# Kernel tuning notes

Hardware: AMD Instinct MI355X
Metric: run time of the kernel (lower is better)

Reference implementation:

```python
import jax, jax.numpy as jnp
import numpy as np

N, H, E, D, L = 100000, 20000, 1600000, 64, 3
F = 4 * D  # ffn hidden = out_dim * 4


def _ln(x, g, b, eps=1e-5):
    mu = x.mean(-1, keepdims=True)
    var = ((x - mu) ** 2).mean(-1, keepdims=True)
    return (x - mu) * jax.lax.rsqrt(var + eps) * g + b


def _gconv(x, W, b, src, dst, inv_sqrt_src, inv_sqrt_dst, n_dst):
    # DGL GraphConv, norm='both': D_dst^{-1/2} A D_src^{-1/2} (x W) + b
    h = (x * inv_sqrt_src[:, None]) @ W
    agg = jax.ops.segment_sum(h[src], dst, num_segments=n_dst)
    return agg * inv_sqrt_dst[:, None] + b


def setup_inputs() -> dict:
    key = jax.random.key(0)
    ks = jax.random.split(key, 24)
    s = 0.05
    inp = {
        'node_features': jax.random.normal(ks[0], (N, D), jnp.float32),
        'edge_src': jax.random.randint(ks[1], (E,), 0, N),
        'edge_dst': jax.random.randint(ks[2], (E,), 0, H),
        'n_hyper': H,
        # stacked per-layer params [L, ...]
        'Wn2h': jax.random.normal(ks[3], (L, D, D), jnp.float32) * s,
        'bn2h': jnp.zeros((L, D), jnp.float32),
        'Wh2n': jax.random.normal(ks[4], (L, D, D), jnp.float32) * s,
        'bh2n': jnp.zeros((L, D), jnp.float32),
        'W1': jax.random.normal(ks[5], (L, D, F), jnp.float32) * s,
        'b1': jnp.zeros((L, F), jnp.float32),
        'W2': jax.random.normal(ks[6], (L, F, D), jnp.float32) * s,
        'b2': jnp.zeros((L, D), jnp.float32),
        'g1': jnp.ones((L, D), jnp.float32),
        'be1': jnp.zeros((L, D), jnp.float32),
        'g2': jnp.ones((L, D), jnp.float32),
        'be2': jnp.zeros((L, D), jnp.float32),
        'gF': jnp.ones((D,), jnp.float32),
        'bF': jnp.zeros((D,), jnp.float32),
        'Wo': jax.random.normal(ks[7], (D, D), jnp.float32) * s,
        'bo': jnp.zeros((D,), jnp.float32),
    }
    return inp


def reference(node_features, edge_src, edge_dst, n_hyper, Wn2h, bn2h, Wh2n, bh2n,
              W1, b1, W2, b2, g1, be1, g2, be2, gF, bF, Wo, bo):
    n_nodes = node_features.shape[0]
    ones = jnp.ones(edge_src.shape[0], node_features.dtype)
    deg_node = jnp.clip(jax.ops.segment_sum(ones, edge_src, num_segments=n_nodes), 1.0)
    deg_hyp = jnp.clip(jax.ops.segment_sum(ones, edge_dst, num_segments=n_hyper), 1.0)
    is_node = jax.lax.rsqrt(deg_node)  # node out-degree^{-1/2}
    is_hyp = jax.lax.rsqrt(deg_hyp)    # hyperedge in-degree^{-1/2}

    def step(h, p):
        Wa, ba, Wb, bb, w1, c1, w2, c2, gg1, ee1, gg2, ee2 = p
        # node -> hyperedge conv (unused attention output is overwritten in the original)
        h_hyper = _gconv(h, Wa, ba, edge_src, edge_dst, is_node, is_hyp, n_hyper)
        # hyperedge -> node conv on reversed graph (degrees swap roles)
        h_node = _gconv(h_hyper, Wb, bb, edge_dst, edge_src, is_hyp, is_node, n_nodes)
        h = _ln(h + h_node, gg1, ee1)
        h_ffn = jax.nn.relu(h @ w1 + c1) @ w2 + c2
        h = _ln(h + h_ffn, gg2, ee2)
        return h, None

    h, _ = jax.lax.scan(step, node_features,
                        (Wn2h, bn2h, Wh2n, bh2n, W1, b1, W2, b2, g1, be1, g2, be2))
    h = _ln(h, gF, bF)
    return h @ Wo + bo
```

## Files before the change

### kernel.cpp

```cpp
#include <hip/hip_runtime.h>

#define HYP 20000
#define NLAYER 3
#define NB_H 313
#define NB_N 391
#define PT 4096

typedef __attribute__((ext_vector_type(8))) short short8;
typedef __attribute__((ext_vector_type(4))) float floatx4;

static __device__ __forceinline__ unsigned short f2bf(float f){
  union { float f; unsigned u; } v; v.f = f;
  unsigned r = v.u + 0x7FFF + ((v.u >> 16) & 1);
  return (unsigned short)(r >> 16);
}

__global__ __launch_bounds__(256) void k_hist(const int* __restrict__ src,
    const int* __restrict__ dst, int E, int* __restrict__ bh, int* __restrict__ bn){
  __shared__ int lh[NB_H + NB_N];
  int tid = threadIdx.x;
  for (int i = tid; i < NB_H + NB_N; i += 256) lh[i] = 0;
  __syncthreads();
  for (int i = blockIdx.x*256 + tid; i < E; i += gridDim.x*256){
    atomicAdd(&lh[dst[i] >> 6], 1);
    atomicAdd(&lh[NB_H + (src[i] >> 8)], 1);
  }
  __syncthreads();
  for (int i = tid; i < NB_H; i += 256) if (lh[i]) atomicAdd(&bh[i], lh[i]);
  for (int i = tid; i < NB_N; i += 256) if (lh[NB_H+i]) atomicAdd(&bn[i], lh[NB_H+i]);
}

__global__ __launch_bounds__(256) void k_bscan(const int* __restrict__ bh,
    const int* __restrict__ bn, int* __restrict__ bstart_h, int* __restrict__ gcur_h,
    int* __restrict__ bstart_n, int* __restrict__ gcur_n){
  __shared__ int ssc[4];
  __shared__ int scarry;
  int tid = threadIdx.x, lane = tid & 63, wv = tid >> 6;
  if (tid == 0) scarry = 0;
  __syncthreads();
  for (int base = 0; base < NB_H; base += 256){
    int i = base + tid; int v = (i < NB_H) ? bh[i] : 0; int x = v;
    #pragma unroll
    for (int o = 1; o < 64; o <<= 1){ int t = __shfl_up(x,o,64); if (lane >= o) x += t; }
    if (lane == 63) ssc[wv] = x;
    __syncthreads();
    int add = (wv>0?ssc[0]:0)+(wv>1?ssc[1]:0)+(wv>2?ssc[2]:0);
    int c = scarry;
    if (i < NB_H){ int ex = c + add + x - v; bstart_h[i] = ex; gcur_h[i] = ex; }
    __syncthreads();
    if (tid == 255) scarry = c + ssc[0]+ssc[1]+ssc[2]+ssc[3];
    __syncthreads();
  }
  if (tid == 0){ bstart_h[NB_H] = scarry; scarry = 0; }
  __syncthreads();
  for (int base = 0; base < NB_N; base += 256){
    int i = base + tid; int v = (i < NB_N) ? bn[i] : 0; int x = v;
    #pragma unroll
    for (int o = 1; o < 64; o <<= 1){ int t = __shfl_up(x,o,64); if (lane >= o) x += t; }
    if (lane == 63) ssc[wv] = x;
    __syncthreads();
    int add = (wv>0?ssc[0]:0)+(wv>1?ssc[1]:0)+(wv>2?ssc[2]:0);
    int c = scarry;
    if (i < NB_N){ int ex = c + add + x - v; bstart_n[i] = ex; gcur_n[i] = ex; }
    __syncthreads();
    if (tid == 255) scarry = c + ssc[0]+ssc[1]+ssc[2]+ssc[3];
    __syncthreads();
  }
  if (tid == 0) bstart_n[NB_N] = scarry;
}

__global__ __launch_bounds__(256) void k_partition2(
    const int* __restrict__ esrc, const int* __restrict__ edst, int E, int nblk,
    int* __restrict__ gcur_h, unsigned* __restrict__ Ebuf_h,
    int* __restrict__ gcur_n, unsigned* __restrict__ Ebuf_n){
  __shared__ unsigned sst[PT];
  __shared__ int lh[NB_N], lpre[NB_N], gb[NB_N];
  __shared__ int ssc[4];
  __shared__ int scarry;
  int tid = threadIdx.x, lane = tid & 63, wv = tid >> 6;
  bool hside = (blockIdx.x < nblk);
  int bb = hside ? blockIdx.x : blockIdx.x - nblk;
  const int* keys = hside ? edst : esrc;
  const int* pays = hside ? esrc : edst;
  int keyshift = hside ? 17 : 15;
  int nb = hside ? NB_H : NB_N;
  int* gcur = hside ? gcur_h : gcur_n;
  unsigned* Ebuf = hside ? Ebuf_h : Ebuf_n;

  int base = bb*PT;
  int m = min(PT, E - base);
  for (int i = tid; i < nb; i += 256) lh[i] = 0;
  if (tid == 0) scarry = 0;
  __syncthreads();
  unsigned en[16]; int rk[16];
  #pragma unroll
  for (int j = 0; j < 16; ++j){
    int i = base + j*256 + tid;
    if (i < E){
      unsigned k = (unsigned)keys[i], p = (unsigned)pays[i];
      en[j] = (k << keyshift) | p;
      rk[j] = atomicAdd(&lh[en[j] >> 23], 1);
    } else { en[j] = 0; rk[j] = -1; }
  }
  __syncthreads();
  for (int b2 = 0; b2 < nb; b2 += 256){
    int i = b2 + tid; int v = (i < nb) ? lh[i] : 0; int x = v;
    #pragma unroll
    for (int o = 1; o < 64; o <<= 1){ int t = __shfl_up(x,o,64); if (lane >= o) x += t; }
    if (lane == 63) ssc[wv] = x;
    __syncthreads();
    int add = (wv>0?ssc[0]:0)+(wv>1?ssc[1]:0)+(wv>2?ssc[2]:0);
    int c = scarry;
    if (i < nb) lpre[i] = c + add + x - v;
    __syncthreads();
    if (tid == 255) scarry = c + ssc[0]+ssc[1]+ssc[2]+ssc[3];
    __syncthreads();
  }
  for (int i = tid; i < nb; i += 256) gb[i] = atomicAdd(&gcur[i], lh[i]);
  #pragma unroll
  for (int j = 0; j < 16; ++j){
    if (rk[j] >= 0){
      int bk = en[j] >> 23;
      sst[lpre[bk] + rk[j]] = en[j];
    }
  }
  __syncthreads();
  for (int j = tid; j < m; j += 256){
    unsigned e = sst[j];
    int bk = e >> 23;
    Ebuf[gb[bk] + (j - lpre[bk])] = e;
  }
}

__global__ __launch_bounds__(256) void k_build2(
    const unsigned* __restrict__ Ebuf_h, const int* __restrict__ bstart_h,
    const unsigned* __restrict__ Ebuf_n, const int* __restrict__ bstart_n,
    int* __restrict__ off_h, float* __restrict__ is_h, int* __restrict__ csr_h,
    int* __restrict__ off_n, float* __restrict__ is_n, int* __restrict__ csr_n,
    const float* __restrict__ nf, unsigned short* __restrict__ xb,
    int Hn, int Nn){
  __shared__ int lcnt[256], lpre2[256], lcur[256];
  int tid = threadIdx.x, lane = tid & 63, wv = tid >> 6;
  bool hside = (blockIdx.x < NB_H);
  int b = hside ? blockIdx.x : blockIdx.x - NB_H;
  const unsigned* Ebuf = hside ? Ebuf_h : Ebuf_n;
  const int* bstart = hside ? bstart_h : bstart_n;
  int keyshift = hside ? 17 : 15;
  int ipb = hside ? 64 : 256;
  int paymask = hside ? 0x1FFFF : 0x7FFF;
  int limit = hside ? Hn : Nn;
  int* off = hside ? off_h : off_n;
  float* isv = hside ? is_h : is_n;
  int* csr = hside ? csr_h : csr_n;

  int base = bstart[b], m = bstart[b+1] - base;
  for (int i = tid; i < ipb; i += 256) lcnt[i] = 0;
  __syncthreads();
  for (int i = tid; i < m; i += 256){
    unsigned e = Ebuf[base + i];
    atomicAdd(&lcnt[(e >> keyshift) & (ipb-1)], 1);
  }
  __syncthreads();
  if (wv == 0){
    int carry = 0;
    for (int c = 0; c < ipb; c += 64){
      int li = c + lane;
      int v = lcnt[li]; int x = v;
      #pragma unroll
      for (int o = 1; o < 64; o <<= 1){ int t = __shfl_up(x,o,64); if (lane >= o) x += t; }
      int ex = carry + x - v;
      int id = b*ipb + li;
      if (id <= limit) off[id] = base + ex;
      if (id < limit) isv[id] = rsqrtf((float)(v > 0 ? v : 1));
      lpre2[li] = ex;
      carry += __shfl(x, 63, 64);
    }
  }
  for (int i = tid; i < ipb; i += 256) lcur[i] = 0;
  __syncthreads();
  for (int i = tid; i < m; i += 256){
    unsigned e = Ebuf[base + i];
    int li = (e >> keyshift) & (ipb-1);
    int pos = base + lpre2[li] + atomicAdd(&lcur[li], 1);
    csr[pos] = (int)(e & (unsigned)paymask);
  }
  if (!hside){
    int nbase = b*256;
    for (int i = tid; i < 2048; i += 256){
      int li = i >> 3, kc = (i & 7)*8;
      int id = nbase + li;
      if (id < Nn){
        int v = lcnt[li];
        float s = rsqrtf((float)(v > 0 ? v : 1));
        float4 v0 = *(const float4*)&nf[(size_t)id*64 + kc];
        float4 v1 = *(const float4*)&nf[(size_t)id*64 + kc + 4];
        uint4 o;
        o.x = (unsigned)f2bf(v0.x*s) | ((unsigned)f2bf(v0.y*s) << 16);
        o.y = (unsigned)f2bf(v0.z*s) | ((unsigned)f2bf(v0.w*s) << 16);
        o.z = (unsigned)f2bf(v1.x*s) | ((unsigned)f2bf(v1.y*s) << 16);
        o.w = (unsigned)f2bf(v1.z*s) | ((unsigned)f2bf(v1.w*s) << 16);
        *(uint4*)&xb[(size_t)id*64 + kc] = o;
      }
    }
  }
}

__global__ void k_cvtall(const float* __restrict__ W1, const float* __restrict__ W2,
                         const float* __restrict__ Wa, const float* __restrict__ Wb,
                         const float* __restrict__ Wo,
                         unsigned short* __restrict__ W1T, unsigned short* __restrict__ W2T,
                         unsigned short* __restrict__ WaT, unsigned short* __restrict__ WbT,
                         unsigned short* __restrict__ WoT){
  int st = gridDim.x*blockDim.x;
  int t0 = blockIdx.x*blockDim.x + threadIdx.x;
  for (int j = t0; j < NLAYER*16384; j += st){
    int l = j >> 14, n = (j >> 6) & 255, k = j & 63;
    W1T[j] = f2bf(W1[l*16384 + k*256 + n]);
  }
  for (int j = t0; j < NLAYER*16384; j += st){
    int l = j >> 14, o = (j >> 8) & 63, kk = j & 255;
    W2T[j] = f2bf(W2[l*16384 + kk*64 + o]);
  }
  for (int j = t0; j < NLAYER*4096; j += st){
    int l = j >> 12, n = (j >> 6) & 63, k = j & 63;
    WaT[j] = f2bf(Wa[l*4096 + k*64 + n]);
  }
  for (int j = t0; j < NLAYER*4096; j += st){
    int l = j >> 12, n = (j >> 6) & 63, k = j & 63;
    WbT[j] = f2bf(Wb[l*4096 + k*64 + n]);
  }
  for (int j = t0; j < 4096; j += st){
    int n = (j >> 6) & 63, k = j & 63;
    WoT[j] = f2bf(Wo[k*64 + n]);
  }
}

template<int LSTR>
static __device__ __forceinline__ void stage64(const unsigned short* __restrict__ gsrc,
    unsigned short* __restrict__ ldst, int tid, int rows){
  int nch = rows*8;
  for (int idx = tid; idx < nch; idx += 256){
    int row = idx >> 3, kc = (idx & 7)*8;
    uint4 v = *(const uint4*)&gsrc[row*64 + kc];
    *(uint4*)&ldst[row*LSTR + kc] = v;
  }
}

static __device__ __forceinline__ short8 rdswz(const unsigned short* __restrict__ l,
    int row, int slot){
  return *(const short8*)&l[(row << 6) + ((((unsigned)(slot ^ row)) & 7u) << 3)];
}

#define ACC8(u) \
  a0 += __uint_as_float(u.x << 16); a1 += __uint_as_float(u.x & 0xFFFF0000u); \
  a2 += __uint_as_float(u.y << 16); a3 += __uint_as_float(u.y & 0xFFFF0000u); \
  a4 += __uint_as_float(u.z << 16); a5 += __uint_as_float(u.z & 0xFFFF0000u); \
  a6 += __uint_as_float(u.w << 16); a7 += __uint_as_float(u.w & 0xFFFF0000u);

#define ACCV(u) \
  a[0] += __uint_as_float(u.x << 16); a[1] += __uint_as_float(u.x & 0xFFFF0000u); \
  a[2] += __uint_as_float(u.y << 16); a[3] += __uint_as_float(u.y & 0xFFFF0000u); \
  a[4] += __uint_as_float(u.z << 16); a[5] += __uint_as_float(u.z & 0xFFFF0000u); \
  a[6] += __uint_as_float(u.w << 16); a[7] += __uint_as_float(u.w & 0xFFFF0000u);

__global__ __launch_bounds__(256) void k_gather8(const unsigned short* __restrict__ feat,
    const int* __restrict__ csr, const int* __restrict__ off,
    unsigned short* __restrict__ agg, int nrows){
  int lane = threadIdx.x & 63, wvi = threadIdx.x >> 6;
  int g = lane >> 3;
  int ch = (lane & 7) * 8;
  int r = blockIdx.x*4 + wvi, stride = gridDim.x*4;
  for (; r < nrows; r += stride){
    int b = off[r], e = off[r+1];
    float a0=0,a1=0,a2=0,a3=0,a4=0,a5=0,a6=0,a7=0;
    int t = b;
    for (; t + 32 <= e; t += 32){
      int s0 = csr[t + g];
      int s1 = csr[t + 8 + g];
      int s2 = csr[t + 16 + g];
      int s3 = csr[t + 24 + g];
      uint4 u0 = *(const uint4*)&feat[(size_t)s0*64 + ch];
      uint4 u1 = *(const uint4*)&feat[(size_t)s1*64 + ch];
      uint4 u2 = *(const uint4*)&feat[(size_t)s2*64 + ch];
      uint4 u3 = *(const uint4*)&feat[(size_t)s3*64 + ch];
      ACC8(u0); ACC8(u1); ACC8(u2); ACC8(u3);
    }
    for (; t + 16 <= e; t += 16){
      int s0 = csr[t + g];
      int s1 = csr[t + 8 + g];
      uint4 u0 = *(const uint4*)&feat[(size_t)s0*64 + ch];
      uint4 u1 = *(const uint4*)&feat[(size_t)s1*64 + ch];
      ACC8(u0); ACC8(u1);
    }
    for (; t < e; t += 8){
      int idx = t + g;
      bool valid = idx < e;
      int s = csr[valid ? idx : b];
      uint4 u = *(const uint4*)&feat[(size_t)s*64 + ch];
      if (!valid){ u.x = 0; u.y = 0; u.z = 0; u.w = 0; }
      ACC8(u);
    }
    #pragma unroll
    for (int o = 8; o <= 32; o <<= 1){
      a0 += __shfl_xor(a0,o,64); a1 += __shfl_xor(a1,o,64);
      a2 += __shfl_xor(a2,o,64); a3 += __shfl_xor(a3,o,64);
      a4 += __shfl_xor(a4,o,64); a5 += __shfl_xor(a5,o,64);
      a6 += __shfl_xor(a6,o,64); a7 += __shfl_xor(a7,o,64);
    }
    if (g == 0){
      uint4 w;
      w.x = (unsigned)f2bf(a0) | ((unsigned)f2bf(a1) << 16);
      w.y = (unsigned)f2bf(a2) | ((unsigned)f2bf(a3) << 16);
      w.z = (unsigned)f2bf(a4) | ((unsigned)f2bf(a5) << 16);
      w.w = (unsigned)f2bf(a6) | ((unsigned)f2bf(a7) << 16);
      *(uint4*)&agg[(size_t)r*64 + ch] = w;
    }
  }
}

__global__ __launch_bounds__(256) void k_gatherN(const unsigned short* __restrict__ feat,
    const int* __restrict__ csr, const int* __restrict__ off,
    unsigned short* __restrict__ agg, int nrows){
  int lane = threadIdx.x & 63, wvi = threadIdx.x >> 6;
  int g = lane >> 3;
  int ch = (lane & 7) * 8;
  int wid = blockIdx.x*4 + wvi;
  int nw = gridDim.x*4;
  for (int r0 = wid*8; r0 < nrows; r0 += nw*8){
    int r = r0 + g;
    bool vr = (r < nrows);
    int b = 0, e = 0;
    if (vr){ b = off[r]; e = off[r+1]; }
    float a[8] = {0,0,0,0,0,0,0,0};
    int t = b;
    for (; t + 2 <= e; t += 2){
      int s0 = csr[t];
      int s1 = csr[t+1];
      uint4 u0 = *(const uint4*)&feat[(size_t)s0*64 + ch];
      uint4 u1 = *(const uint4*)&feat[(size_t)s1*64 + ch];
      ACCV(u0); ACCV(u1);
    }
    if (t < e){
      int s = csr[t];
      uint4 u = *(const uint4*)&feat[(size_t)s*64 + ch];
      ACCV(u);
    }
    if (vr){
      uint4 w;
      w.x = (unsigned)f2bf(a[0]) | ((unsigned)f2bf(a[1]) << 16);
      w.y = (unsigned)f2bf(a[2]) | ((unsigned)f2bf(a[3]) << 16);
      w.z = (unsigned)f2bf(a[4]) | ((unsigned)f2bf(a[5]) << 16);
      w.w = (unsigned)f2bf(a[6]) | ((unsigned)f2bf(a[7]) << 16);
      *(uint4*)&agg[(size_t)r*64 + ch] = w;
    }
  }
}

__global__ __launch_bounds__(64) void k_mmA(const unsigned short* __restrict__ aggb,
    const unsigned short* __restrict__ WaT, const float* __restrict__ bias,
    const float* __restrict__ ihy, unsigned short* __restrict__ ouths, int nrows){
  __shared__ unsigned short sWb[64*72];
  int lane = threadIdx.x;
  int quad = lane >> 4, n16 = lane & 15;
  for (int idx = lane; idx < 512; idx += 64){
    int row = idx >> 3, kc = (idx & 7)*8;
    *(uint4*)&sWb[row*72 + kc] = *(const uint4*)&WaT[row*64 + kc];
  }
  __syncthreads();
  int rowbase = blockIdx.x*16;
  int arow = min(rowbase + n16, nrows-1);
  short8 a0 = *(const short8*)&aggb[(size_t)arow*64 + quad*8];
  short8 a1 = *(const short8*)&aggb[(size_t)arow*64 + 32 + quad*8];
  float ih[4];
  #pragma unroll
  for (int r = 0; r < 4; ++r) ih[r] = ihy[min(rowbase + quad*4 + r, nrows-1)];
  #pragma unroll
  for (int ot = 0; ot < 4; ++ot){
    floatx4 c = (floatx4){0.f,0.f,0.f,0.f};
    short8 b0 = *(const short8*)&sWb[(ot*16+n16)*72 + quad*8];
    short8 b1 = *(const short8*)&sWb[(ot*16+n16)*72 + 32 + quad*8];
    c = __builtin_amdgcn_mfma_f32_16x16x32_bf16(a0, b0, c, 0, 0, 0);
    c = __builtin_amdgcn_mfma_f32_16x16x32_bf16(a1, b1, c, 0, 0, 0);
    float bl = bias[ot*16 + n16];
    #pragma unroll
    for (int r = 0; r < 4; ++r){
      int rr = rowbase + quad*4 + r;
      if (rr < nrows)
        ouths[(size_t)rr*64 + ot*16 + n16] = f2bf(fmaf(c[r], ih[r], bl) * ih[r]);
    }
  }
}

__global__ __launch_bounds__(1024) void k_fused(
    const unsigned short* __restrict__ aggb,
    const unsigned short* __restrict__ WbT,
    const float* __restrict__ bbg,
    const float* __restrict__ isn,
    const float* __restrict__ hin,
    const float* __restrict__ g1v, const float* __restrict__ be1v,
    const unsigned short* __restrict__ W1T, const float* __restrict__ b1g,
    const unsigned short* __restrict__ W2T, const float* __restrict__ b2g,
    const float* __restrict__ g2v, const float* __restrict__ be2v,
    float* __restrict__ Outp, unsigned short* __restrict__ Qs, int nrows)
{
  __shared__ unsigned short sWb[64*64];
  __shared__ unsigned short sW1[4*64*64];
  __shared__ unsigned short sW2[4*64*64];
  __shared__ unsigned short sPH[16*16*72];
  int tid = threadIdx.x;
  int lane = tid & 63, w = tid >> 6;
  int quad = lane >> 4, n16 = lane & 15;
  unsigned short* myP = &sPH[w*16*72];

  for (int c = tid; c < 4608; c += 1024){
    int tile = c >> 9, cc = c & 511;
    int row = cc >> 3, s = cc & 7;
    const unsigned short* src; unsigned short* dst; int gs;
    if (tile == 0){ src = WbT; gs = 64; dst = sWb; }
    else if (tile < 5){ int q = tile-1; src = W1T + q*64*64; gs = 64; dst = sW1 + q*4096; }
    else { int q = tile-5; src = W2T + q*64; gs = 256; dst = sW2 + q*4096; }
    uint4 v = *(const uint4*)&src[row*gs + s*8];
    *(uint4*)&dst[(row << 6) + ((((unsigned)(s ^ row)) & 7u) << 3)] = v;
  }

  float bbv[4], g1l[4], be1l[4], b2v[4], g2l[4], be2l[4];
  #pragma unroll
  for (int ot = 0; ot < 4; ++ot){
    bbv[ot] = bbg[ot*16 + n16];
    g1l[ot] = g1v[ot*16 + n16];  be1l[ot] = be1v[ot*16 + n16];
    b2v[ot] = b2g[ot*16 + n16];
    g2l[ot] = g2v[ot*16 + n16];  be2l[ot] = be2v[ot*16 + n16];
  }
  float b1v[4][4];
  #pragma unroll
  for (int q = 0; q < 4; ++q)
    #pragma unroll
    for (int c2 = 0; c2 < 4; ++c2)
      b1v[q][c2] = b1g[q*64 + c2*16 + n16];

  __syncthreads();

  int ngrp = (nrows + 15) >> 4;
  int wwid = blockIdx.x*16 + w;
  int nw = gridDim.x*16;

  for (int grp = wwid; grp < ngrp; grp += nw){
    int rb = grp*16;

    int arow = min(rb + n16, nrows-1);
    short8 a0 = *(const short8*)&aggb[(size_t)arow*64 + quad*8];
    short8 a1 = *(const short8*)&aggb[(size_t)arow*64 + 32 + quad*8];

    float pP[4][4];
    float isr[4];
    #pragma unroll
    for (int r = 0; r < 4; ++r) isr[r] = isn[min(rb + quad*4 + r, nrows-1)];
    #pragma unroll
    for (int ot = 0; ot < 4; ++ot){
      floatx4 c = (floatx4){0.f,0.f,0.f,0.f};
      short8 b0 = rdswz(sWb, ot*16+n16, quad);
      short8 b1 = rdswz(sWb, ot*16+n16, 4+quad);
      c = __builtin_amdgcn_mfma_f32_16x16x32_bf16(a0, b0, c, 0, 0, 0);
      c = __builtin_amdgcn_mfma_f32_16x16x32_bf16(a1, b1, c, 0, 0, 0);
      #pragma unroll
      for (int r = 0; r < 4; ++r){
        int rr = min(rb + quad*4 + r, nrows-1);
        pP[ot][r] = fmaf(c[r], isr[r], bbv[ot]) + hin[(size_t)rr*64 + ot*16 + n16];
      }
    }
    #pragma unroll
    for (int r = 0; r < 4; ++r){
      float sv = (pP[0][r] + pP[1][r]) + (pP[2][r] + pP[3][r]);
      float q = fmaf(pP[0][r], pP[0][r], pP[1][r]*pP[1][r]) +
                fmaf(pP[2][r], pP[2][r], pP[3][r]*pP[3][r]);
      #pragma unroll
      for (int o = 8; o >= 1; o >>= 1){
        sv += __shfl_xor(sv, o, 64);
        q  += __shfl_xor(q, o, 64);
      }
      float mu = sv*(1.f/64.f);
      float var = fmaf(-mu, mu, q*(1.f/64.f));
      float rs = rsqrtf(var + 1e-5f);
      #pragma unroll
      for (int ot = 0; ot < 4; ++ot)
        pP[ot][r] = fmaf((pP[ot][r]-mu)*rs, g1l[ot], be1l[ot]);
    }
    #pragma unroll
    for (int ot = 0; ot < 4; ++ot)
      #pragma unroll
      for (int r = 0; r < 4; ++r)
        myP[(quad*4 + r)*72 + ot*16 + n16] = f2bf(pP[ot][r]);
    short8 p0 = *(const short8*)&myP[n16*72 + quad*8];
    short8 p1 = *(const short8*)&myP[n16*72 + 32 + quad*8];

    floatx4 acc2[4];
    #pragma unroll
    for (int t = 0; t < 4; ++t) acc2[t] = (floatx4){0.f,0.f,0.f,0.f};

    #pragma unroll
    for (int q = 0; q < 4; ++q){
      const unsigned short* sA = sW1 + q*4096;
      const unsigned short* sB = sW2 + q*4096;
      #pragma unroll
      for (int ck2 = 0; ck2 < 2; ++ck2){
        #pragma unroll
        for (int nt = 0; nt < 2; ++nt){
          int nl = ck2*32 + nt*16 + n16;
          floatx4 c = (floatx4){0.f,0.f,0.f,0.f};
          short8 b0 = rdswz(sA, nl, quad);
          short8 b1f = rdswz(sA, nl, 4+quad);
          c = __builtin_amdgcn_mfma_f32_16x16x32_bf16(p0, b0, c, 0, 0, 0);
          c = __builtin_amdgcn_mfma_f32_16x16x32_bf16(p1, b1f, c, 0, 0, 0);
          float bb = b1v[q][ck2*2 + nt];
          #pragma unroll
          for (int r = 0; r < 4; ++r){
            float h = fmaxf(c[r] + bb, 0.f);
            myP[(quad*4 + r)*40 + nt*16 + n16] = f2bf(h);
          }
        }
        short8 a2 = *(const short8*)&myP[n16*40 + quad*8];
        #pragma unroll
        for (int ot = 0; ot < 4; ++ot){
          short8 b2f = rdswz(sB, ot*16+n16, ck2*4 + quad);
          acc2[ot] = __builtin_amdgcn_mfma_f32_16x16x32_bf16(a2, b2f, acc2[ot], 0, 0, 0);
        }
      }
    }

    float pre[4][4];
    #pragma unroll
    for (int ot = 0; ot < 4; ++ot)
      #pragma unroll
      for (int r = 0; r < 4; ++r)
        pre[ot][r] = acc2[ot][r] + b2v[ot] + pP[ot][r];
    #pragma unroll
    for (int r = 0; r < 4; ++r){
      float sv = (pre[0][r] + pre[1][r]) + (pre[2][r] + pre[3][r]);
      float q = fmaf(pre[0][r], pre[0][r], pre[1][r]*pre[1][r]) +
                fmaf(pre[2][r], pre[2][r], pre[3][r]*pre[3][r]);
      #pragma unroll
      for (int o = 8; o >= 1; o >>= 1){
        sv += __shfl_xor(sv, o, 64);
        q  += __shfl_xor(q, o, 64);
      }
      float mu = sv*(1.f/64.f);
      float var = fmaf(-mu, mu, q*(1.f/64.f));
      float rs = rsqrtf(var + 1e-5f);
      int rr = rb + quad*4 + r;
      if (rr < nrows){
        float isr2 = isn[rr];
        #pragma unroll
        for (int ot = 0; ot < 4; ++ot){
          float ov = fmaf((pre[ot][r]-mu)*rs, g2l[ot], be2l[ot]);
          Outp[(size_t)rr*64 + ot*16 + n16] = ov;
          Qs[(size_t)rr*64 + ot*16 + n16] = f2bf(ov * isr2);
        }
      }
    }
  }
}

__global__ __launch_bounds__(256) void k_final(const float* __restrict__ Q,
    const unsigned short* __restrict__ WoT, const float* __restrict__ bog,
    const float* __restrict__ gF, const float* __restrict__ bF,
    float* __restrict__ out, int nrows){
  __shared__ unsigned short sWb[64*72];
  int tid = threadIdx.x;
  int lane = tid & 63, w = tid >> 6;
  int quad = lane >> 4, n16 = lane & 15;
  stage64<72>(WoT, sWb, tid, 64);
  __syncthreads();
  int rowbase = blockIdx.x*64 + w*16;
  int arow = min(rowbase + n16, nrows-1);
  float4 q0 = *(const float4*)&Q[(size_t)arow*64 + quad*8];
  float4 q1 = *(const float4*)&Q[(size_t)arow*64 + quad*8 + 4];
  float4 q2 = *(const float4*)&Q[(size_t)arow*64 + 32 + quad*8];
  float4 q3 = *(const float4*)&Q[(size_t)arow*64 + 32 + quad*8 + 4];
  float s = (q0.x+q0.y+q0.z+q0.w) + (q1.x+q1.y+q1.z+q1.w)
          + (q2.x+q2.y+q2.z+q2.w) + (q3.x+q3.y+q3.z+q3.w);
  float qq = (q0.x*q0.x+q0.y*q0.y+q0.z*q0.z+q0.w*q0.w)
           + (q1.x*q1.x+q1.y*q1.y+q1.z*q1.z+q1.w*q1.w)
           + (q2.x*q2.x+q2.y*q2.y+q2.z*q2.z+q2.w*q2.w)
           + (q3.x*q3.x+q3.y*q3.y+q3.z*q3.z+q3.w*q3.w);
  s += __shfl_xor(s, 16, 64);  qq += __shfl_xor(qq, 16, 64);
  s += __shfl_xor(s, 32, 64);  qq += __shfl_xor(qq, 32, 64);
  float mu = s*(1.f/64.f);
  float var = fmaf(-mu, mu, qq*(1.f/64.f));
  float rs = rsqrtf(var + 1e-5f);
  float4 g0 = *(const float4*)&gF[quad*8];
  float4 g1 = *(const float4*)&gF[quad*8 + 4];
  float4 g2 = *(const float4*)&gF[32 + quad*8];
  float4 g3 = *(const float4*)&gF[32 + quad*8 + 4];
  float4 f0 = *(const float4*)&bF[quad*8];
  float4 f1 = *(const float4*)&bF[quad*8 + 4];
  float4 f2 = *(const float4*)&bF[32 + quad*8];
  float4 f3 = *(const float4*)&bF[32 + quad*8 + 4];
  short8 a0, a1;
  a0[0]=f2bf(fmaf((q0.x-mu)*rs, g0.x, f0.x)); a0[1]=f2bf(fmaf((q0.y-mu)*rs, g0.y, f0.y));
  a0[2]=f2bf(fmaf((q0.z-mu)*rs, g0.z, f0.z)); a0[3]=f2bf(fmaf((q0.w-mu)*rs, g0.w, f0.w));
  a0[4]=f2bf(fmaf((q1.x-mu)*rs, g1.x, f1.x)); a0[5]=f2bf(fmaf((q1.y-mu)*rs, g1.y, f1.y));
  a0[6]=f2bf(fmaf((q1.z-mu)*rs, g1.z, f1.z)); a0[7]=f2bf(fmaf((q1.w-mu)*rs, g1.w, f1.w));
  a1[0]=f2bf(fmaf((q2.x-mu)*rs, g2.x, f2.x)); a1[1]=f2bf(fmaf((q2.y-mu)*rs, g2.y, f2.y));
  a1[2]=f2bf(fmaf((q2.z-mu)*rs, g2.z, f2.z)); a1[3]=f2bf(fmaf((q2.w-mu)*rs, g2.w, f2.w));
  a1[4]=f2bf(fmaf((q3.x-mu)*rs, g3.x, f3.x)); a1[5]=f2bf(fmaf((q3.y-mu)*rs, g3.y, f3.y));
  a1[6]=f2bf(fmaf((q3.z-mu)*rs, g3.z, f3.z)); a1[7]=f2bf(fmaf((q3.w-mu)*rs, g3.w, f3.w));
  #pragma unroll
  for (int ot = 0; ot < 4; ++ot){
    floatx4 c = (floatx4){0.f,0.f,0.f,0.f};
    short8 b0 = *(const short8*)&sWb[(ot*16+n16)*72 + quad*8];
    short8 b1 = *(const short8*)&sWb[(ot*16+n16)*72 + 32 + quad*8];
    c = __builtin_amdgcn_mfma_f32_16x16x32_bf16(a0, b0, c, 0, 0, 0);
    c = __builtin_amdgcn_mfma_f32_16x16x32_bf16(a1, b1, c, 0, 0, 0);
    float bol = bog[ot*16 + n16];
    #pragma unroll
    for (int r = 0; r < 4; ++r){
      int rr = rowbase + quad*4 + r;
      if (rr < nrows) out[(size_t)rr*64 + ot*16 + n16] = c[r] + bol;
    }
  }
}

extern "C" void kernel_launch(void* const* d_in, const int* in_sizes, int n_in,
                              void* d_out, int out_size, void* d_ws, size_t ws_size,
                              hipStream_t stream){
  const float* nf   = (const float*)d_in[0];
  const int*   esrc = (const int*)d_in[1];
  const int*   edst = (const int*)d_in[2];
  const float* Wn2h = (const float*)d_in[4];
  const float* bn2h = (const float*)d_in[5];
  const float* Wh2n = (const float*)d_in[6];
  const float* bh2n = (const float*)d_in[7];
  const float* W1   = (const float*)d_in[8];
  const float* b1   = (const float*)d_in[9];
  const float* W2   = (const float*)d_in[10];
  const float* b2   = (const float*)d_in[11];
  const float* g1   = (const float*)d_in[12];
  const float* be1  = (const float*)d_in[13];
  const float* g2   = (const float*)d_in[14];
  const float* be2  = (const float*)d_in[15];
  const float* gF   = (const float*)d_in[16];
  const float* bF   = (const float*)d_in[17];
  const float* Wo   = (const float*)d_in[18];
  const float* bo   = (const float*)d_in[19];
  const int N = in_sizes[0] / 64;
  const int E = in_sizes[1];
  const int H = HYP;
  float* out = (float*)d_out;

  char* w = (char*)d_ws;
  auto carve = [&](size_t bytes) -> char* {
    char* p = w; w += (bytes + 255) & ~(size_t)255; return p;
  };
  int* bh = (int*)carve((size_t)(NB_H + NB_N)*4);
  int* bn = bh + NB_H;
  int* bstart_h = (int*)carve((size_t)(NB_H+1)*4);
  int* gcur_h   = (int*)carve((size_t)NB_H*4);
  int* bstart_n = (int*)carve((size_t)(NB_N+1)*4);
  int* gcur_n   = (int*)carve((size_t)NB_N*4);
  unsigned* Ebuf_h = (unsigned*)carve((size_t)E*4);
  unsigned* Ebuf_n = (unsigned*)carve((size_t)E*4);
  int*   off_h = (int*)carve((size_t)(H+1)*4);
  int*   off_n = (int*)carve((size_t)(N+1)*4);
  float* is_h  = (float*)carve((size_t)H*4);
  float* is_n  = (float*)carve((size_t)N*4);
  int*   csr_h = (int*)carve((size_t)E*4);
  int*   csr_n = (int*)carve((size_t)E*4);
  unsigned short* aggxb = (unsigned short*)carve((size_t)H*64*2);
  unsigned short* agghb = (unsigned short*)carve((size_t)N*64*2);
  float* Qb    = (float*)carve((size_t)N*64*4);
  unsigned short* hhsb = (unsigned short*)carve((size_t)H*64*2);
  unsigned short* xb0  = (unsigned short*)carve((size_t)N*64*2);
  unsigned short* Qs   = (unsigned short*)carve((size_t)N*64*2);
  unsigned short* W1g16 = (unsigned short*)carve((size_t)NLAYER*64*256*2);
  unsigned short* W2g16 = (unsigned short*)carve((size_t)NLAYER*256*64*2);
  unsigned short* Wag16 = (unsigned short*)carve((size_t)NLAYER*4096*2);
  unsigned short* Wbg16 = (unsigned short*)carve((size_t)NLAYER*4096*2);
  unsigned short* Wog16 = (unsigned short*)carve((size_t)4096*2);

  hipMemsetAsync(bh, 0, (size_t)(NB_H + NB_N)*4, stream);
  k_cvtall<<<96, 256, 0, stream>>>(W1, W2, Wn2h, Wh2n, Wo,
                                   W1g16, W2g16, Wag16, Wbg16, Wog16);
  k_hist<<<512, 256, 0, stream>>>(esrc, edst, E, bh, bn);
  k_bscan<<<1, 256, 0, stream>>>(bh, bn, bstart_h, gcur_h, bstart_n, gcur_n);
  const int nblk = (E + PT - 1)/PT;
  k_partition2<<<2*nblk, 256, 0, stream>>>(esrc, edst, E, nblk,
                                           gcur_h, Ebuf_h, gcur_n, Ebuf_n);
  k_build2<<<NB_H + NB_N, 256, 0, stream>>>(Ebuf_h, bstart_h, Ebuf_n, bstart_n,
                                            off_h, is_h, csr_h,
                                            off_n, is_n, csr_n,
                                            nf, xb0, H, N);

  const int NB64 = (N + 63)/64;
  const int HB16 = (H + 15)/16;
  for (int l = 0; l < NLAYER; ++l){
    const float* hin = (l == 0) ? nf : Qb;
    const unsigned short* hsrc = (l == 0) ? xb0 : Qs;
    k_gather8<<<2048, 256, 0, stream>>>(hsrc, csr_h, off_h, aggxb, H);
    k_mmA<<<HB16, 64, 0, stream>>>(aggxb, Wag16 + l*4096, bn2h + l*64, is_h, hhsb, H);
    k_gatherN<<<2048, 256, 0, stream>>>(hhsb, csr_n, off_n, agghb, N);
    k_fused<<<256, 1024, 0, stream>>>(agghb, Wbg16 + l*4096, bh2n + l*64, is_n, hin,
                                      g1 + l*64, be1 + l*64,
                                      W1g16 + l*64*256, b1 + l*256,
                                      W2g16 + l*256*64, b2 + l*64,
                                      g2 + l*64, be2 + l*64, Qb, Qs, N);
  }
  k_final<<<NB64, 256, 0, stream>>>(Qb, Wog16, bo, gF, bF, out, N);
}
```

Before: 457.4 us.

## Fuse both GraphConv weight matmuls into the hyperedge gather kernel

Since aggregation is linear, the hyperedge-to-node weight Wb is applied per hyperedge before the node-side gather instead of after it. The new gather kernel also applies Wa, the bias and the degree scaling with scalar FMAs against LDS-held bf16 weights. This removes the separate k_mmA launch, its bf16 intermediate and the Wb MFMA in k_fused, and Wa/Wb are no longer pre-converted in k_cvtall. In exchange the hyperedge output is stored as fp32, so the heavy node-side gather reads twice as many bytes per edge. Every gather block also converts both weight matrices into LDS, and k_fused now reads bf16 aggregates with scalar 2-byte loads.

```diff
diff --git a/kernel.cpp b/kernel.cpp
--- a/kernel.cpp
+++ b/kernel.cpp
@@ -206,10 +206,8 @@
 }
 
 __global__ void k_cvtall(const float* __restrict__ W1, const float* __restrict__ W2,
-                         const float* __restrict__ Wa, const float* __restrict__ Wb,
                          const float* __restrict__ Wo,
                          unsigned short* __restrict__ W1T, unsigned short* __restrict__ W2T,
-                         unsigned short* __restrict__ WaT, unsigned short* __restrict__ WbT,
                          unsigned short* __restrict__ WoT){
   int st = gridDim.x*blockDim.x;
   int t0 = blockIdx.x*blockDim.x + threadIdx.x;
@@ -220,14 +218,6 @@
   for (int j = t0; j < NLAYER*16384; j += st){
     int l = j >> 14, o = (j >> 8) & 63, kk = j & 255;
     W2T[j] = f2bf(W2[l*16384 + kk*64 + o]);
-  }
-  for (int j = t0; j < NLAYER*4096; j += st){
-    int l = j >> 12, n = (j >> 6) & 63, k = j & 63;
-    WaT[j] = f2bf(Wa[l*4096 + k*64 + n]);
-  }
-  for (int j = t0; j < NLAYER*4096; j += st){
-    int l = j >> 12, n = (j >> 6) & 63, k = j & 63;
-    WbT[j] = f2bf(Wb[l*4096 + k*64 + n]);
   }
   for (int j = t0; j < 4096; j += st){
     int n = (j >> 6) & 63, k = j & 63;
@@ -251,28 +241,51 @@
   return *(const short8*)&l[(row << 6) + ((((unsigned)(slot ^ row)) & 7u) << 3)];
 }
 
-#define ACC8(u) \
-  a0 += __uint_as_float(u.x << 16); a1 += __uint_as_float(u.x & 0xFFFF0000u); \
-  a2 += __uint_as_float(u.y << 16); a3 += __uint_as_float(u.y & 0xFFFF0000u); \
-  a4 += __uint_as_float(u.z << 16); a5 += __uint_as_float(u.z & 0xFFFF0000u); \
-  a6 += __uint_as_float(u.w << 16); a7 += __uint_as_float(u.w & 0xFFFF0000u);
-
 #define ACCV(u) \
   a[0] += __uint_as_float(u.x << 16); a[1] += __uint_as_float(u.x & 0xFFFF0000u); \
   a[2] += __uint_as_float(u.y << 16); a[3] += __uint_as_float(u.y & 0xFFFF0000u); \
   a[4] += __uint_as_float(u.z << 16); a[5] += __uint_as_float(u.z & 0xFFFF0000u); \
   a[6] += __uint_as_float(u.w << 16); a[7] += __uint_as_float(u.w & 0xFFFF0000u);
 
-__global__ __launch_bounds__(256) void k_gather8(const unsigned short* __restrict__ feat,
-    const int* __restrict__ csr, const int* __restrict__ off,
-    unsigned short* __restrict__ agg, int nrows){
-  int lane = threadIdx.x & 63, wvi = threadIdx.x >> 6;
-  int g = lane >> 3;
-  int ch = (lane & 7) * 8;
+#define ACCF(ua, ub) \
+  a[0] += ua.x; a[1] += ua.y; a[2] += ua.z; a[3] += ua.w; \
+  a[4] += ub.x; a[5] += ub.y; a[6] += ub.z; a[7] += ub.w;
+
+#define MV8(acc, s, wv_) \
+  acc[0] = fmaf(s, __uint_as_float(wv_.x << 16), acc[0]); \
+  acc[1] = fmaf(s, __uint_as_float(wv_.x & 0xFFFF0000u), acc[1]); \
+  acc[2] = fmaf(s, __uint_as_float(wv_.y << 16), acc[2]); \
+  acc[3] = fmaf(s, __uint_as_float(wv_.y & 0xFFFF0000u), acc[3]); \
+  acc[4] = fmaf(s, __uint_as_float(wv_.z << 16), acc[4]); \
+  acc[5] = fmaf(s, __uint_as_float(wv_.z & 0xFFFF0000u), acc[5]); \
+  acc[6] = fmaf(s, __uint_as_float(wv_.w << 16), acc[6]); \
+  acc[7] = fmaf(s, __uint_as_float(wv_.w & 0xFFFF0000u), acc[7]);
+
+__global__ __launch_bounds__(256) void k_gatherHW(
+    const unsigned short* __restrict__ feat, const int* __restrict__ csr,
+    const int* __restrict__ off, const float* __restrict__ Waf,
+    const float* __restrict__ bav_g, const float* __restrict__ Wbf,
+    const float* __restrict__ ihy, float* __restrict__ zb, int nrows){
+  __shared__ unsigned short sWa[64*72];
+  __shared__ unsigned short sWb[64*72];
+  int tid = threadIdx.x;
+  for (int idx = tid; idx < 4096; idx += 256){
+    int k = idx >> 6, j = idx & 63;
+    sWa[k*72 + j] = f2bf(Waf[idx]);
+    sWb[k*72 + j] = f2bf(Wbf[idx]);
+  }
+  int lane = tid & 63, wvi = tid >> 6;
+  int g = lane >> 3, i8 = lane & 7;
+  int ch = i8*8;
+  float bav[8];
+  #pragma unroll
+  for (int m = 0; m < 8; ++m) bav[m] = bav_g[g*8 + m];
+  __syncthreads();
+
   int r = blockIdx.x*4 + wvi, stride = gridDim.x*4;
   for (; r < nrows; r += stride){
     int b = off[r], e = off[r+1];
-    float a0=0,a1=0,a2=0,a3=0,a4=0,a5=0,a6=0,a7=0;
+    float a[8] = {0,0,0,0,0,0,0,0};
     int t = b;
     for (; t + 32 <= e; t += 32){
       int s0 = csr[t + g];
@@ -283,14 +296,14 @@
       uint4 u1 = *(const uint4*)&feat[(size_t)s1*64 + ch];
       uint4 u2 = *(const uint4*)&feat[(size_t)s2*64 + ch];
       uint4 u3 = *(const uint4*)&feat[(size_t)s3*64 + ch];
-      ACC8(u0); ACC8(u1); ACC8(u2); ACC8(u3);
+      ACCV(u0); ACCV(u1); ACCV(u2); ACCV(u3);
     }
     for (; t + 16 <= e; t += 16){
       int s0 = csr[t + g];
       int s1 = csr[t + 8 + g];
       uint4 u0 = *(const uint4*)&feat[(size_t)s0*64 + ch];
       uint4 u1 = *(const uint4*)&feat[(size_t)s1*64 + ch];
-      ACC8(u0); ACC8(u1);
+      ACCV(u0); ACCV(u1);
     }
     for (; t < e; t += 8){
       int idx = t + g;
@@ -298,27 +311,51 @@
       int s = csr[valid ? idx : b];
       uint4 u = *(const uint4*)&feat[(size_t)s*64 + ch];
       if (!valid){ u.x = 0; u.y = 0; u.z = 0; u.w = 0; }
-      ACC8(u);
+      ACCV(u);
     }
     #pragma unroll
     for (int o = 8; o <= 32; o <<= 1){
-      a0 += __shfl_xor(a0,o,64); a1 += __shfl_xor(a1,o,64);
-      a2 += __shfl_xor(a2,o,64); a3 += __shfl_xor(a3,o,64);
-      a4 += __shfl_xor(a4,o,64); a5 += __shfl_xor(a5,o,64);
-      a6 += __shfl_xor(a6,o,64); a7 += __shfl_xor(a7,o,64);
+      #pragma unroll
+      for (int m = 0; m < 8; ++m) a[m] += __shfl_xor(a[m], o, 64);
+    }
+    float ih = ihy[r];
+    float p[8] = {0,0,0,0,0,0,0,0};
+    #pragma unroll
+    for (int tt = 0; tt < 8; ++tt){
+      uint4 wv_ = *(const uint4*)&sWa[(i8*8 + tt)*72 + g*8];
+      float at = a[tt];
+      MV8(p, at, wv_);
+    }
+    #pragma unroll
+    for (int o = 1; o <= 4; o <<= 1){
+      #pragma unroll
+      for (int m = 0; m < 8; ++m) p[m] += __shfl_xor(p[m], o, 64);
+    }
+    float hh[8];
+    #pragma unroll
+    for (int m = 0; m < 8; ++m) hh[m] = fmaf(p[m], ih, bav[m]) * ih;
+    float q[8] = {0,0,0,0,0,0,0,0};
+    #pragma unroll
+    for (int tt = 0; tt < 8; ++tt){
+      uint4 wv_ = *(const uint4*)&sWb[(g*8 + tt)*72 + i8*8];
+      float ht = hh[tt];
+      MV8(q, ht, wv_);
+    }
+    #pragma unroll
+    for (int o = 8; o <= 32; o <<= 1){
+      #pragma unroll
+      for (int m = 0; m < 8; ++m) q[m] += __shfl_xor(q[m], o, 64);
     }
     if (g == 0){
-      uint4 w;
-      w.x = (unsigned)f2bf(a0) | ((unsigned)f2bf(a1) << 16);
-      w.y = (unsigned)f2bf(a2) | ((unsigned)f2bf(a3) << 16);
-      w.z = (unsigned)f2bf(a4) | ((unsigned)f2bf(a5) << 16);
-      w.w = (unsigned)f2bf(a6) | ((unsigned)f2bf(a7) << 16);
-      *(uint4*)&agg[(size_t)r*64 + ch] = w;
-    }
-  }
-}
-
-__global__ __launch_bounds__(256) void k_gatherN(const unsigned short* __restrict__ feat,
+      float4 w0; w0.x = q[0]; w0.y = q[1]; w0.z = q[2]; w0.w = q[3];
+      float4 w1; w1.x = q[4]; w1.y = q[5]; w1.z = q[6]; w1.w = q[7];
+      *(float4*)&zb[(size_t)r*64 + ch] = w0;
+      *(float4*)&zb[(size_t)r*64 + ch + 4] = w1;
+    }
+  }
+}
+
+__global__ __launch_bounds__(256) void k_gatherN(const float* __restrict__ feat,
     const int* __restrict__ csr, const int* __restrict__ off,
     unsigned short* __restrict__ agg, int nrows){
   int lane = threadIdx.x & 63, wvi = threadIdx.x >> 6;
@@ -336,14 +373,17 @@
     for (; t + 2 <= e; t += 2){
       int s0 = csr[t];
       int s1 = csr[t+1];
-      uint4 u0 = *(const uint4*)&feat[(size_t)s0*64 + ch];
-      uint4 u1 = *(const uint4*)&feat[(size_t)s1*64 + ch];
-      ACCV(u0); ACCV(u1);
+      float4 u0a = *(const float4*)&feat[(size_t)s0*64 + ch];
+      float4 u0b = *(const float4*)&feat[(size_t)s0*64 + ch + 4];
+      float4 u1a = *(const float4*)&feat[(size_t)s1*64 + ch];
+      float4 u1b = *(const float4*)&feat[(size_t)s1*64 + ch + 4];
+      ACCF(u0a, u0b); ACCF(u1a, u1b);
     }
     if (t < e){
       int s = csr[t];
-      uint4 u = *(const uint4*)&feat[(size_t)s*64 + ch];
-      ACCV(u);
+      float4 ua = *(const float4*)&feat[(size_t)s*64 + ch];
+      float4 ub = *(const float4*)&feat[(size_t)s*64 + ch + 4];
+      ACCF(ua, ub);
     }
     if (vr){
       uint4 w;
@@ -356,44 +396,8 @@
   }
 }
 
-__global__ __launch_bounds__(64) void k_mmA(const unsigned short* __restrict__ aggb,
-    const unsigned short* __restrict__ WaT, const float* __restrict__ bias,
-    const float* __restrict__ ihy, unsigned short* __restrict__ ouths, int nrows){
-  __shared__ unsigned short sWb[64*72];
-  int lane = threadIdx.x;
-  int quad = lane >> 4, n16 = lane & 15;
-  for (int idx = lane; idx < 512; idx += 64){
-    int row = idx >> 3, kc = (idx & 7)*8;
-    *(uint4*)&sWb[row*72 + kc] = *(const uint4*)&WaT[row*64 + kc];
-  }
-  __syncthreads();
-  int rowbase = blockIdx.x*16;
-  int arow = min(rowbase + n16, nrows-1);
-  short8 a0 = *(const short8*)&aggb[(size_t)arow*64 + quad*8];
-  short8 a1 = *(const short8*)&aggb[(size_t)arow*64 + 32 + quad*8];
-  float ih[4];
-  #pragma unroll
-  for (int r = 0; r < 4; ++r) ih[r] = ihy[min(rowbase + quad*4 + r, nrows-1)];
-  #pragma unroll
-  for (int ot = 0; ot < 4; ++ot){
-    floatx4 c = (floatx4){0.f,0.f,0.f,0.f};
-    short8 b0 = *(const short8*)&sWb[(ot*16+n16)*72 + quad*8];
-    short8 b1 = *(const short8*)&sWb[(ot*16+n16)*72 + 32 + quad*8];
-    c = __builtin_amdgcn_mfma_f32_16x16x32_bf16(a0, b0, c, 0, 0, 0);
-    c = __builtin_amdgcn_mfma_f32_16x16x32_bf16(a1, b1, c, 0, 0, 0);
-    float bl = bias[ot*16 + n16];
-    #pragma unroll
-    for (int r = 0; r < 4; ++r){
-      int rr = rowbase + quad*4 + r;
-      if (rr < nrows)
-        ouths[(size_t)rr*64 + ot*16 + n16] = f2bf(fmaf(c[r], ih[r], bl) * ih[r]);
-    }
-  }
-}
-
 __global__ __launch_bounds__(1024) void k_fused(
     const unsigned short* __restrict__ aggb,
-    const unsigned short* __restrict__ WbT,
     const float* __restrict__ bbg,
     const float* __restrict__ isn,
     const float* __restrict__ hin,
@@ -403,7 +407,6 @@
     const float* __restrict__ g2v, const float* __restrict__ be2v,
     float* __restrict__ Outp, unsigned short* __restrict__ Qs, int nrows)
 {
-  __shared__ unsigned short sWb[64*64];
   __shared__ unsigned short sW1[4*64*64];
   __shared__ unsigned short sW2[4*64*64];
   __shared__ unsigned short sPH[16*16*72];
@@ -412,13 +415,12 @@
   int quad = lane >> 4, n16 = lane & 15;
   unsigned short* myP = &sPH[w*16*72];
 
-  for (int c = tid; c < 4608; c += 1024){
+  for (int c = tid; c < 4096; c += 1024){
     int tile = c >> 9, cc = c & 511;
     int row = cc >> 3, s = cc & 7;
     const unsigned short* src; unsigned short* dst; int gs;
-    if (tile == 0){ src = WbT; gs = 64; dst = sWb; }
-    else if (tile < 5){ int q = tile-1; src = W1T + q*64*64; gs = 64; dst = sW1 + q*4096; }
-    else { int q = tile-5; src = W2T + q*64; gs = 256; dst = sW2 + q*4096; }
+    if (tile < 4){ src = W1T + tile*64*64; gs = 64; dst = sW1 + tile*4096; }
+    else { int q = tile-4; src = W2T + q*64; gs = 256; dst = sW2 + q*4096; }
     uint4 v = *(const uint4*)&src[row*gs + s*8];
     *(uint4*)&dst[(row << 6) + ((((unsigned)(s ^ row)) & 7u) << 3)] = v;
   }
@@ -447,25 +449,17 @@
   for (int grp = wwid; grp < ngrp; grp += nw){
     int rb = grp*16;
 
-    int arow = min(rb + n16, nrows-1);
-    short8 a0 = *(const short8*)&aggb[(size_t)arow*64 + quad*8];
-    short8 a1 = *(const short8*)&aggb[(size_t)arow*64 + 32 + quad*8];
-
     float pP[4][4];
     float isr[4];
     #pragma unroll
     for (int r = 0; r < 4; ++r) isr[r] = isn[min(rb + quad*4 + r, nrows-1)];
     #pragma unroll
     for (int ot = 0; ot < 4; ++ot){
-      floatx4 c = (floatx4){0.f,0.f,0.f,0.f};
-      short8 b0 = rdswz(sWb, ot*16+n16, quad);
-      short8 b1 = rdswz(sWb, ot*16+n16, 4+quad);
-      c = __builtin_amdgcn_mfma_f32_16x16x32_bf16(a0, b0, c, 0, 0, 0);
-      c = __builtin_amdgcn_mfma_f32_16x16x32_bf16(a1, b1, c, 0, 0, 0);
       #pragma unroll
       for (int r = 0; r < 4; ++r){
         int rr = min(rb + quad*4 + r, nrows-1);
-        pP[ot][r] = fmaf(c[r], isr[r], bbv[ot]) + hin[(size_t)rr*64 + ot*16 + n16];
+        float zf = __uint_as_float(((unsigned)aggb[(size_t)rr*64 + ot*16 + n16]) << 16);
+        pP[ot][r] = fmaf(zf, isr[r], bbv[ot]) + hin[(size_t)rr*64 + ot*16 + n16];
       }
     }
     #pragma unroll
@@ -665,21 +659,17 @@
   float* is_n  = (float*)carve((size_t)N*4);
   int*   csr_h = (int*)carve((size_t)E*4);
   int*   csr_n = (int*)carve((size_t)E*4);
-  unsigned short* aggxb = (unsigned short*)carve((size_t)H*64*2);
+  float* zbf   = (float*)carve((size_t)H*64*4);
   unsigned short* agghb = (unsigned short*)carve((size_t)N*64*2);
   float* Qb    = (float*)carve((size_t)N*64*4);
-  unsigned short* hhsb = (unsigned short*)carve((size_t)H*64*2);
   unsigned short* xb0  = (unsigned short*)carve((size_t)N*64*2);
   unsigned short* Qs   = (unsigned short*)carve((size_t)N*64*2);
   unsigned short* W1g16 = (unsigned short*)carve((size_t)NLAYER*64*256*2);
   unsigned short* W2g16 = (unsigned short*)carve((size_t)NLAYER*256*64*2);
-  unsigned short* Wag16 = (unsigned short*)carve((size_t)NLAYER*4096*2);
-  unsigned short* Wbg16 = (unsigned short*)carve((size_t)NLAYER*4096*2);
   unsigned short* Wog16 = (unsigned short*)carve((size_t)4096*2);
 
   hipMemsetAsync(bh, 0, (size_t)(NB_H + NB_N)*4, stream);
-  k_cvtall<<<96, 256, 0, stream>>>(W1, W2, Wn2h, Wh2n, Wo,
-                                   W1g16, W2g16, Wag16, Wbg16, Wog16);
+  k_cvtall<<<96, 256, 0, stream>>>(W1, W2, Wo, W1g16, W2g16, Wog16);
   k_hist<<<512, 256, 0, stream>>>(esrc, edst, E, bh, bn);
   k_bscan<<<1, 256, 0, stream>>>(bh, bn, bstart_h, gcur_h, bstart_n, gcur_n);
   const int nblk = (E + PT - 1)/PT;
@@ -691,14 +681,14 @@
                                             nf, xb0, H, N);
 
   const int NB64 = (N + 63)/64;
-  const int HB16 = (H + 15)/16;
   for (int l = 0; l < NLAYER; ++l){
     const float* hin = (l == 0) ? nf : Qb;
     const unsigned short* hsrc = (l == 0) ? xb0 : Qs;
-    k_gather8<<<2048, 256, 0, stream>>>(hsrc, csr_h, off_h, aggxb, H);
-    k_mmA<<<HB16, 64, 0, stream>>>(aggxb, Wag16 + l*4096, bn2h + l*64, is_h, hhsb, H);
-    k_gatherN<<<2048, 256, 0, stream>>>(hhsb, csr_n, off_n, agghb, N);
-    k_fused<<<256, 1024, 0, stream>>>(agghb, Wbg16 + l*4096, bh2n + l*64, is_n, hin,
+    k_gatherHW<<<2048, 256, 0, stream>>>(hsrc, csr_h, off_h,
+                                         Wn2h + l*4096, bn2h + l*64, Wh2n + l*4096,
+                                         is_h, zbf, H);
+    k_gatherN<<<2048, 256, 0, stream>>>(zbf, csr_n, off_n, agghb, N);
+    k_fused<<<256, 1024, 0, stream>>>(agghb, bh2n + l*64, is_n, hin,
                                       g1 + l*64, be1 + l*64,
                                       W1g16 + l*64*256, b1 + l*256,
                                       W2g16 + l*256*64, b2 + l*64,
```

After: 552.4 us. +20.8%, slower.
